# Optimization experiments

Hardware: AMD Instinct MI355X
Metric: run time of the kernel (lower is better)

Reference implementation:

```python
import jax, jax.numpy as jnp
import numpy as np

N = 50000    # nodes
E = 800000   # edges (avg degree 16)
B = 256      # graphs in the batch (static for segment ops)
H = 128      # feature / hidden width (channels[-2])
NL = 4       # LSTM layers in Set2Set
PS = 4       # Set2Set processing steps
OUT = 2      # channels[-1]


def _bn(h, g, b):
    # BatchNorm1d with batch statistics (training-mode math, biased variance)
    m = h.mean(0)
    v = jnp.mean((h - m) ** 2, 0)
    return (h - m) * jax.lax.rsqrt(v + 1e-5) * g + b


def _gin(x, src, dst, W1, b1, ga1, be1, W2, b2, ga2, be2):
    # GINConv, eps=0: out = MLP(x + sum_{j->i} x_j)
    agg = jax.ops.segment_sum(x[src], dst, num_segments=x.shape[0])
    h = x + agg
    h = jax.nn.relu(_bn(h @ W1.T + b1, ga1, be1))
    h = jax.nn.relu(_bn(h @ W2.T + b2, ga2, be2))
    return h


def _set2set(x, batch, Wih0, Whh0, b0, WihR, WhhR, bR):
    hs = [jnp.zeros((B, H), x.dtype)] * NL
    cs = [jnp.zeros((B, H), x.dtype)] * NL
    q_star = jnp.zeros((B, 2 * H), x.dtype)
    for _ in range(PS):
        inp = q_star
        nhs, ncs = [], []
        for l in range(NL):  # stacked LSTM cells, seq-len 1 per step
            Wih = Wih0 if l == 0 else WihR[l - 1]
            Whh = Whh0 if l == 0 else WhhR[l - 1]
            bb = b0 if l == 0 else bR[l - 1]
            gates = inp @ Wih.T + hs[l] @ Whh.T + bb
            i, f, g, o = jnp.split(gates, 4, axis=-1)  # torch gate order i,f,g,o
            c = jax.nn.sigmoid(f) * cs[l] + jax.nn.sigmoid(i) * jnp.tanh(g)
            h = jax.nn.sigmoid(o) * jnp.tanh(c)
            nhs.append(h); ncs.append(c)
            inp = h
        hs, cs = nhs, ncs
        q = inp  # (B, H) top-layer hidden
        # per-graph segment softmax attention
        e = jnp.sum(x * q[batch], -1)                        # (N,)
        m = jax.ops.segment_max(e, batch, num_segments=B)
        ee = jnp.exp(e - m[batch])
        s = jax.ops.segment_sum(ee, batch, num_segments=B)
        a = ee / s[batch]
        r = jax.ops.segment_sum(a[:, None] * x, batch, num_segments=B)  # (B, H)
        q_star = jnp.concatenate([q, r], -1)
    return q_star


def setup_inputs() -> dict:
    key = jax.random.key(0)
    ks = jax.random.split(key, 16)

    def w(k, shape):
        return jax.random.normal(k, shape, jnp.float32) * 0.05

    d = {}
    d["x"] = jax.random.normal(ks[0], (N, H), jnp.float32)
    d["edge_index"] = jax.random.randint(ks[1], (2, E), 0, N, dtype=jnp.int32)
    d["batch"] = jnp.sort(jax.random.randint(ks[2], (N,), 0, B, dtype=jnp.int32))
    for i, g in enumerate(("g0", "g1")):
        kk = jax.random.split(ks[3 + i], 2)
        d[g + "_W1"] = w(kk[0], (H, H)); d[g + "_b1"] = jnp.zeros((H,), jnp.float32)
        d[g + "_gamma1"] = jnp.ones((H,), jnp.float32); d[g + "_beta1"] = jnp.zeros((H,), jnp.float32)
        d[g + "_W2"] = w(kk[1], (H, H)); d[g + "_b2"] = jnp.zeros((H,), jnp.float32)
        d[g + "_gamma2"] = jnp.ones((H,), jnp.float32); d[g + "_beta2"] = jnp.zeros((H,), jnp.float32)
    d["Wih0"] = w(ks[6], (4 * H, 2 * H))
    d["Whh0"] = w(ks[7], (4 * H, H))
    d["b0"] = jnp.zeros((4 * H,), jnp.float32)
    d["WihR"] = w(ks[8], (NL - 1, 4 * H, H))
    d["WhhR"] = w(ks[9], (NL - 1, 4 * H, H))
    d["bR"] = jnp.zeros((NL - 1, 4 * H), jnp.float32)
    d["lin_W"] = w(ks[10], (OUT, 2 * H))
    d["lin_b"] = jnp.zeros((OUT,), jnp.float32)
    return d


def reference(x, edge_index, batch,
              g0_W1, g0_b1, g0_gamma1, g0_beta1, g0_W2, g0_b2, g0_gamma2, g0_beta2,
              g1_W1, g1_b1, g1_gamma1, g1_beta1, g1_W2, g1_b2, g1_gamma2, g1_beta2,
              Wih0, Whh0, b0, WihR, WhhR, bR, lin_W, lin_b):
    src, dst = edge_index[0], edge_index[1]
    x = _gin(x, src, dst, g0_W1, g0_b1, g0_gamma1, g0_beta1, g0_W2, g0_b2, g0_gamma2, g0_beta2)
    x = _gin(x, src, dst, g1_W1, g1_b1, g1_gamma1, g1_beta1, g1_W2, g1_b2, g1_gamma2, g1_beta2)
    q = _set2set(x, batch, Wih0, Whh0, b0, WihR, WhhR, bR)
    # F.dropout(p=0.1) is identity in eval mode
    return q @ lin_W.T + lin_b
```

## Files before the change

### kernel.cpp

```cpp
#include <hip/hip_runtime.h>
#include <math.h>

#define NN 50000
#define EE 800000
#define BBG 256
#define HHC 128
#define SEG_CAP 448
#define ESC 512
#define NBIN 196
#define NBLK 196

typedef _Float16 half8 __attribute__((ext_vector_type(8)));
typedef _Float16 half4 __attribute__((ext_vector_type(4)));
typedef _Float16 half2v __attribute__((ext_vector_type(2)));
typedef float f32x4 __attribute__((ext_vector_type(4)));

#if defined(__has_builtin)
#if __has_builtin(__builtin_amdgcn_fdot2)
#define USE_FDOT2 1
#endif
#endif

__device__ __forceinline__ float fdot2f(half2v a, half2v b, float c) {
#ifdef USE_FDOT2
  return __builtin_amdgcn_fdot2(a, b, c, false);
#else
  return fmaf((float)a[0], (float)b[0], fmaf((float)a[1], (float)b[1], c));
#endif
}

__device__ __forceinline__ float fsigm(float x) {
  return __builtin_amdgcn_rcpf(1.f + __expf(-x));
}
__device__ __forceinline__ float ftanh(float x) {
  return 1.f - 2.f * __builtin_amdgcn_rcpf(1.f + __expf(2.f * x));
}

__device__ __forceinline__ float4 aff4(float4 v, float4 sc, float4 sh) {
  v.x = fmaxf(fmaf(v.x, sc.x, sh.x), 0.f);
  v.y = fmaxf(fmaf(v.y, sc.y, sh.y), 0.f);
  v.z = fmaxf(fmaf(v.z, sc.z, sh.z), 0.f);
  v.w = fmaxf(fmaf(v.w, sc.w, sh.w), 0.f);
  return v;
}

__global__ __launch_bounds__(256) void prep_all_kernel(
    const int* __restrict__ batch,
    const int* __restrict__ ei,
    const float* __restrict__ W0, const float* __restrict__ W1,
    const float* __restrict__ W2, const float* __restrict__ W3,
    const float* __restrict__ Wih0, const float* __restrict__ Whh0,
    const float* __restrict__ WihR, const float* __restrict__ WhhR,
    const float* __restrict__ b0, const float* __restrict__ bR,
    const float* __restrict__ xsrc,
    float* __restrict__ stats, int* __restrict__ gptr, int* __restrict__ partial,
    _Float16* __restrict__ ginWh, _Float16* __restrict__ WT0h,
    _Float16* __restrict__ WTRh, float* __restrict__ bc0, float* __restrict__ bcR,
    _Float16* __restrict__ x16a) {
  __shared__ int hist[NBIN];
  int blk = blockIdx.x, tid = threadIdx.x;
  if (blk == 0) {
    ((float4*)stats)[tid] = make_float4(0.f, 0.f, 0.f, 0.f);
    return;
  }
  if (blk <= 196) {
    int i = (blk - 1) * 256 + tid;
    if (i >= NN) return;
    int b = batch[i];
    int prev = (i == 0) ? -1 : batch[i - 1];
    for (int g = prev + 1; g <= b; ++g) gptr[g] = i;
    if (i == NN - 1) {
      for (int g = b + 1; g <= BBG; ++g) gptr[g] = NN;
    }
    return;
  }
  if (blk <= 392) {
    int b = blk - 197;
    if (tid < NBIN) hist[tid] = 0;
    __syncthreads();
    const int4* dst4 = (const int4*)(ei + EE);
#pragma unroll
    for (int c = 0; c < 4; ++c) {
      int idx = b * 1024 + c * 256 + tid;
      if (idx < EE / 4) {
        int4 d = dst4[idx];
        atomicAdd(&hist[d.x >> 8], 1);
        atomicAdd(&hist[d.y >> 8], 1);
        atomicAdd(&hist[d.z >> 8], 1);
        atomicAdd(&hist[d.w >> 8], 1);
      }
    }
    __syncthreads();
    if (tid < NBIN) partial[tid * NBLK + b] = hist[tid];
    return;
  }
  if (blk >= 2961) {
    int i = (blk - 2961) * 256 + tid;
    float4 v = ((const float4*)xsrc)[i];
    half4 h;
    h[0] = (_Float16)v.x; h[1] = (_Float16)v.y;
    h[2] = (_Float16)v.z; h[3] = (_Float16)v.w;
    ((half4*)x16a)[i] = h;
    return;
  }
  int idx = (blk - 393) * 256 + tid;
  if (idx < 65536) {
    int m = idx >> 14;
    int r = idx & 16383;
    const float* W = (m == 0) ? W0 : (m == 1) ? W1 : (m == 2) ? W2 : W3;
    ginWh[idx] = (_Float16)W[r];
  } else if (idx < 262144) {
    int t = idx - 65536;
    int k = t >> 9, op = t & 511;
    int j = op >> 2, g = op & 3;
    int row = g * 128 + j;
    float v = (k < 256) ? Wih0[row * 256 + k] : Whh0[row * 128 + (k - 256)];
    WT0h[((k >> 1) << 10) | (op << 1) | (k & 1)] = (_Float16)v;
  } else if (idx < 655360) {
    int t = idx - 262144;
    int l = t >> 17;
    int rem = t & 131071;
    int k = rem >> 9, op = rem & 511;
    int j = op >> 2, g = op & 3;
    int row = g * 128 + j;
    float v = (k < 128) ? WihR[((size_t)l * 512 + row) * 128 + k]
                        : WhhR[((size_t)l * 512 + row) * 128 + (k - 128)];
    WTRh[((size_t)l << 17) | ((k >> 1) << 10) | (op << 1) | (k & 1)] = (_Float16)v;
  } else {
    int t = idx - 655360;
    if (t < 512) {
      bc0[t] = b0[(t & 3) * 128 + (t >> 2)];
    } else {
      int u = t - 512;
      int l = u >> 9, op = u & 511;
      bcR[u] = bR[l * 512 + (op & 3) * 128 + (op >> 2)];
    }
  }
}


__global__ void scan_partials_kernel(const int* __restrict__ partial,
                                     int* __restrict__ block_base, int* __restrict__ total) {
  __shared__ int buf[256];
  int bin = blockIdx.x, tid = threadIdx.x;
  int v = (tid < NBLK) ? partial[bin * NBLK + tid] : 0;
  buf[tid] = v;
  __syncthreads();
  for (int off = 1; off < 256; off <<= 1) {
    int t = (tid >= off) ? buf[tid - off] : 0;
    __syncthreads();
    buf[tid] += t;
    __syncthreads();
  }
  if (tid < NBLK) block_base[bin * NBLK + tid] = buf[tid] - v;
  if (tid == 255) total[bin] = buf[255];
}

__global__ void scan_totals_kernel(const int* __restrict__ total, int* __restrict__ coarse_base) {
  __shared__ int buf[256];
  int tid = threadIdx.x;
  int v = (tid < NBIN) ? total[tid] : 0;
  buf[tid] = v;
  __syncthreads();
  for (int off = 1; off < 256; off <<= 1) {
    int t = (tid >= off) ? buf[tid - off] : 0;
    __syncthreads();
    buf[tid] += t;
    __syncthreads();
  }
  if (tid < NBIN) coarse_base[tid] = buf[tid] - v;
  if (tid == 255) coarse_base[NBIN] = buf[255];
}

__global__ __launch_bounds__(256) void bucket_scatter_kernel(const int* __restrict__ ei,
                                                             const int* __restrict__ coarse_base,
                                                             const int* __restrict__ block_base,
                                                             int* __restrict__ packed) {
  __shared__ int cursor[NBIN];
  int tid = threadIdx.x, b = blockIdx.x;
  if (tid < NBIN) cursor[tid] = coarse_base[tid] + block_base[tid * NBLK + b];
  __syncthreads();
  const int4* src4 = (const int4*)ei;
  const int4* dst4 = (const int4*)(ei + EE);
#pragma unroll
  for (int c = 0; c < 4; ++c) {
    int idx = b * 1024 + c * 256 + tid;
    if (idx < EE / 4) {
      int4 s = src4[idx];
      int4 d = dst4[idx];
      int p;
      p = atomicAdd(&cursor[d.x >> 8], 1); packed[p] = (s.x << 8) | (d.x & 255);
      p = atomicAdd(&cursor[d.y >> 8], 1); packed[p] = (s.y << 8) | (d.y & 255);
      p = atomicAdd(&cursor[d.z >> 8], 1); packed[p] = (s.z << 8) | (d.z & 255);
      p = atomicAdd(&cursor[d.w >> 8], 1); packed[p] = (s.w << 8) | (d.w & 255);
    }
  }
}

__global__ __launch_bounds__(256) void csr_finalize_kernel(const int* __restrict__ packed,
                                                           const int* __restrict__ coarse_base,
                                                           int* __restrict__ row_start,
                                                           int* __restrict__ csr) {
  __shared__ int fh[256];
  __shared__ int fb[256];
  int bin = blockIdx.x, tid = threadIdx.x;
  int e0 = coarse_base[bin], e1 = coarse_base[bin + 1];
  fh[tid] = 0;
  __syncthreads();
  for (int e = e0 + tid; e < e1; e += 256) atomicAdd(&fh[packed[e] & 255], 1);
  __syncthreads();
  int v = fh[tid];
  fb[tid] = v;
  __syncthreads();
  for (int off = 1; off < 256; off <<= 1) {
    int t = (tid >= off) ? fb[tid - off] : 0;
    __syncthreads();
    fb[tid] += t;
    __syncthreads();
  }
  int excl = fb[tid] - v;
  int node = bin * 256 + tid;
  if (node < NN) row_start[node] = e0 + excl;
  if (bin == NBIN - 1 && tid == 0) row_start[NN] = EE;
  __syncthreads();
  fb[tid] = excl;
  __syncthreads();
  for (int e = e0 + tid; e < e1; e += 256) {
    int p = packed[e];
    int pos = atomicAdd(&fb[p & 255], 1);
    csr[e0 + pos] = p >> 8;
  }
}

template <bool AFF>
__device__ __forceinline__ void acc8(float* acc, half8 h, const float* scv,
                                     const float* shv) {
#pragma unroll
  for (int f = 0; f < 8; ++f) {
    float v = (float)h[f];
    if (AFF) v = fmaxf(fmaf(v, scv[f], shv[f]), 0.f);
    acc[f] += v;
  }
}

template <bool AFF>
__global__ __launch_bounds__(256) void gin_agg_kernel(
    const _Float16* __restrict__ x16, const int* __restrict__ row_start,
    const int* __restrict__ csr,
    const float* __restrict__ stats, const float* __restrict__ gamma,
    const float* __restrict__ beta, _Float16* __restrict__ outp) {
  __shared__ float sc_s[128], sh_s[128];
  if (AFF) {
    int tt = threadIdx.x;
    if (tt < 128) {
      const float invN = 1.0f / (float)NN;
      float mm = stats[tt] * invN;
      float vv = stats[128 + tt] * invN - mm * mm;
      float rs = rsqrtf(vv + 1e-5f);
      float sc = gamma[tt] * rs;
      sc_s[tt] = sc;
      sh_s[tt] = beta[tt] - mm * sc;
    }
    __syncthreads();
  }
  int node = blockIdx.x * 16 + (threadIdx.x >> 4);
  int t = threadIdx.x & 15;
  const half8* xh8 = (const half8*)x16;
  float scv[8], shv[8];
  if (AFF) {
#pragma unroll
    for (int f = 0; f < 8; ++f) { scv[f] = sc_s[t * 8 + f]; shv[f] = sh_s[t * 8 + f]; }
  }
  int s0 = row_start[node], s1 = row_start[node + 1];
  float acc[8] = {0.f, 0.f, 0.f, 0.f, 0.f, 0.f, 0.f, 0.f};
  int j = s0;
  for (; j + 8 <= s1; j += 8) {
    int i0 = csr[j + 0];
    int i1 = csr[j + 1];
    int i2 = csr[j + 2];
    int i3 = csr[j + 3];
    int i4 = csr[j + 4];
    int i5 = csr[j + 5];
    int i6 = csr[j + 6];
    int i7 = csr[j + 7];
    half8 h0 = xh8[(size_t)i0 * 16 + t];
    half8 h1 = xh8[(size_t)i1 * 16 + t];
    half8 h2 = xh8[(size_t)i2 * 16 + t];
    half8 h3 = xh8[(size_t)i3 * 16 + t];
    half8 h4 = xh8[(size_t)i4 * 16 + t];
    half8 h5 = xh8[(size_t)i5 * 16 + t];
    half8 h6 = xh8[(size_t)i6 * 16 + t];
    half8 h7 = xh8[(size_t)i7 * 16 + t];
    acc8<AFF>(acc, h0, scv, shv);
    acc8<AFF>(acc, h1, scv, shv);
    acc8<AFF>(acc, h2, scv, shv);
    acc8<AFF>(acc, h3, scv, shv);
    acc8<AFF>(acc, h4, scv, shv);
    acc8<AFF>(acc, h5, scv, shv);
    acc8<AFF>(acc, h6, scv, shv);
    acc8<AFF>(acc, h7, scv, shv);
  }
  if (j + 4 <= s1) {
    int i0 = csr[j + 0];
    int i1 = csr[j + 1];
    int i2 = csr[j + 2];
    int i3 = csr[j + 3];
    half8 h0 = xh8[(size_t)i0 * 16 + t];
    half8 h1 = xh8[(size_t)i1 * 16 + t];
    half8 h2 = xh8[(size_t)i2 * 16 + t];
    half8 h3 = xh8[(size_t)i3 * 16 + t];
    acc8<AFF>(acc, h0, scv, shv);
    acc8<AFF>(acc, h1, scv, shv);
    acc8<AFF>(acc, h2, scv, shv);
    acc8<AFF>(acc, h3, scv, shv);
    j += 4;
  }
  for (; j < s1; ++j) {
    int i = csr[j];
    half8 h = xh8[(size_t)i * 16 + t];
    acc8<AFF>(acc, h, scv, shv);
  }
  half8 selfh = xh8[(size_t)node * 16 + t];
  half8 hv;
#pragma unroll
  for (int f = 0; f < 8; ++f) {
    float sv = (float)selfh[f];
    if (AFF) sv = fmaxf(fmaf(sv, scv[f], shv[f]), 0.f);
    hv[f] = (_Float16)(acc[f] + sv);
  }
  ((half8*)outp)[(size_t)node * 16 + t] = hv;
}

template <bool BN, bool AH>
__global__ __launch_bounds__(256) void gemm_gin_mfma_kernel(
    const float* __restrict__ A, const _Float16* __restrict__ A16,
    const _Float16* __restrict__ Wh,
    const float* __restrict__ bias,
    const float* __restrict__ stats, const float* __restrict__ gamma,
    const float* __restrict__ beta,
    float* __restrict__ C, _Float16* __restrict__ h16out,
    float* __restrict__ ssum, float* __restrict__ ssq) {
  __shared__ float bsc_s[128], bsh_s[128];
  int tid = threadIdx.x;
  if (BN) {
    if (tid < 128) {
      const float invN = 1.0f / (float)NN;
      float mm = stats[tid] * invN;
      float vv = stats[128 + tid] * invN - mm * mm;
      float rs = rsqrtf(vv + 1e-5f);
      float sc = gamma[tid] * rs;
      bsc_s[tid] = sc;
      bsh_s[tid] = beta[tid] - mm * sc;
    }
    __syncthreads();
  }
  int w = tid >> 6, l = tid & 63;
  int lr = l & 15, lg = l >> 4;
  int cb = w * 32;
  half8 bf0[4], bf1[4];
#pragma unroll
  for (int ks = 0; ks < 4; ++ks) {
    int k = ks * 32 + lg * 8;
    bf0[ks] = *(const half8*)(Wh + (size_t)(cb + lr) * 128 + k);
    bf1[ks] = *(const half8*)(Wh + (size_t)(cb + 16 + lr) * 128 + k);
  }
  float bv0 = bias[cb + lr], bv1 = bias[cb + 16 + lr];
  float ps0 = 0.f, pq0 = 0.f, ps1 = 0.f, pq1 = 0.f;
  int t0 = blockIdx.x * 4;
  for (int t = 0; t < 4; ++t) {
    int tile = t0 + t;
    if (tile >= 3125) break;
    int r = tile * 16 + lr;
    half8 af[4];
#pragma unroll
    for (int ks = 0; ks < 4; ++ks) {
      int k0 = ks * 32 + lg * 8;
      if constexpr (AH) {
        half8 ah = *(const half8*)(A16 + (size_t)r * 128 + k0);
        if constexpr (BN) {
          float4 s0 = *(const float4*)&bsc_s[k0];
          float4 s1 = *(const float4*)&bsc_s[k0 + 4];
          float4 h0 = *(const float4*)&bsh_s[k0];
          float4 h1 = *(const float4*)&bsh_s[k0 + 4];
          half8 o;
          o[0] = (_Float16)fmaxf(fmaf((float)ah[0], s0.x, h0.x), 0.f);
          o[1] = (_Float16)fmaxf(fmaf((float)ah[1], s0.y, h0.y), 0.f);
          o[2] = (_Float16)fmaxf(fmaf((float)ah[2], s0.z, h0.z), 0.f);
          o[3] = (_Float16)fmaxf(fmaf((float)ah[3], s0.w, h0.w), 0.f);
          o[4] = (_Float16)fmaxf(fmaf((float)ah[4], s1.x, h1.x), 0.f);
          o[5] = (_Float16)fmaxf(fmaf((float)ah[5], s1.y, h1.y), 0.f);
          o[6] = (_Float16)fmaxf(fmaf((float)ah[6], s1.z, h1.z), 0.f);
          o[7] = (_Float16)fmaxf(fmaf((float)ah[7], s1.w, h1.w), 0.f);
          af[ks] = o;
        } else {
          af[ks] = ah;
        }
      } else {
        float4 a0 = *(const float4*)(A + (size_t)r * 128 + k0);
        float4 a1 = *(const float4*)(A + (size_t)r * 128 + k0 + 4);
        if constexpr (BN) {
          float4 s0 = *(const float4*)&bsc_s[k0];
          float4 s1 = *(const float4*)&bsc_s[k0 + 4];
          float4 h0 = *(const float4*)&bsh_s[k0];
          float4 h1 = *(const float4*)&bsh_s[k0 + 4];
          a0 = aff4(a0, s0, h0);
          a1 = aff4(a1, s1, h1);
        }
        half8 o;
        o[0] = (_Float16)a0.x; o[1] = (_Float16)a0.y;
        o[2] = (_Float16)a0.z; o[3] = (_Float16)a0.w;
        o[4] = (_Float16)a1.x; o[5] = (_Float16)a1.y;
        o[6] = (_Float16)a1.z; o[7] = (_Float16)a1.w;
        af[ks] = o;
      }
    }
    f32x4 acc0 = {0.f, 0.f, 0.f, 0.f};
    f32x4 acc1 = {0.f, 0.f, 0.f, 0.f};
#pragma unroll
    for (int ks = 0; ks < 4; ++ks) {
      acc0 = __builtin_amdgcn_mfma_f32_16x16x32_f16(af[ks], bf0[ks], acc0, 0, 0, 0);
      acc1 = __builtin_amdgcn_mfma_f32_16x16x32_f16(af[ks], bf1[ks], acc1, 0, 0, 0);
    }
#pragma unroll
    for (int i = 0; i < 4; ++i) {
      int rr = tile * 16 + lg * 4 + i;
      float v0 = acc0[i] + bv0;
      float v1 = acc1[i] + bv1;
      if (C) {
        C[(size_t)rr * 128 + cb + lr] = v0;
        C[(size_t)rr * 128 + cb + 16 + lr] = v1;
      }
      if (h16out) {
        h16out[(size_t)rr * 128 + cb + lr] = (_Float16)v0;
        h16out[(size_t)rr * 128 + cb + 16 + lr] = (_Float16)v1;
      }
      ps0 += v0; pq0 += v0 * v0;
      ps1 += v1; pq1 += v1 * v1;
    }
  }
  ps0 += __shfl_xor(ps0, 16); ps0 += __shfl_xor(ps0, 32);
  pq0 += __shfl_xor(pq0, 16); pq0 += __shfl_xor(pq0, 32);
  ps1 += __shfl_xor(ps1, 16); ps1 += __shfl_xor(ps1, 32);
  pq1 += __shfl_xor(pq1, 16); pq1 += __shfl_xor(pq1, 32);
  if (lg == 0) {
    atomicAdd(&ssum[cb + lr], ps0);
    atomicAdd(&ssq[cb + lr], pq0);
    atomicAdd(&ssum[cb + 16 + lr], ps1);
    atomicAdd(&ssq[cb + 16 + lr], pq1);
  }
}

__global__ void __launch_bounds__(1024) set2set_kernel(
    const _Float16* __restrict__ x, const int* __restrict__ gptr,
    const float* __restrict__ stats, const float* __restrict__ gamma,
    const float* __restrict__ beta,
    const _Float16* __restrict__ WT0h, const _Float16* __restrict__ WTRh,
    const float* __restrict__ bc0, const float* __restrict__ bcR,
    float* __restrict__ ebuf,
    const float* __restrict__ linW, const float* __restrict__ linb,
    float* __restrict__ out) {
  __shared__ half2v xs[SEG_CAP * 64];
  __shared__ float wpart[16][512];
  __shared__ half2v inp2[192];
  __shared__ float hcs[4][128];
  __shared__ float ccs[4][128];
  __shared__ float qst[256];
  __shared__ float es[ESC];
  __shared__ float bsc[128], bsh[128];
  __shared__ float wred[16];
  __shared__ float smax_s, ssum_s;
  __shared__ float fred[2][4];

  int g = blockIdx.x, tid = threadIdx.x;
  int w16 = tid >> 6, lane = tid & 63;

  if (tid < 128) {
    const float invN = 1.0f / (float)NN;
    float mm = stats[tid] * invN;
    float vv = stats[128 + tid] * invN - mm * mm;
    float rs = rsqrtf(vv + 1e-5f);
    float sc = gamma[tid] * rs;
    bsc[tid] = sc;
    bsh[tid] = beta[tid] - mm * sc;
#pragma unroll
    for (int l = 0; l < 4; ++l) { hcs[l][tid] = 0.f; ccs[l][tid] = 0.f; }
  }
  if (tid < 256) qst[tid] = 0.f;
  __syncthreads();

  int s0 = gptr[g], s1 = gptr[g + 1];
  int seg = s1 - s0;
  int ncache = seg < SEG_CAP ? seg : SEG_CAP;
  const half2v* xh = (const half2v*)x;
  float sc0 = bsc[2 * lane], sc1 = bsc[2 * lane + 1];
  float sh0 = bsh[2 * lane], sh1 = bsh[2 * lane + 1];
  for (int n = w16; n < ncache; n += 16) {
    half2v v = xh[(size_t)(s0 + n) * 64 + lane];
    half2v h;
    h[0] = (_Float16)fmaxf(fmaf((float)v[0], sc0, sh0), 0.f);
    h[1] = (_Float16)fmaxf(fmaf((float)v[1], sc1, sh1), 0.f);
    xs[n * 64 + lane] = h;
  }
  __syncthreads();

  int s_ = tid >> 6, cg = tid & 63;

  for (int step = 0; step < 4; ++step) {
    for (int cell = 0; cell < 4; ++cell) {
      const _Float16* WTh; const float* bias; int KP2;
      if (cell == 0) {
        WTh = WT0h; bias = bc0; KP2 = 12;
        if (tid < 192) {
          int k = tid << 1;
          float va, vb;
          if (k < 256) { va = qst[k]; vb = qst[k + 1]; }
          else { va = hcs[0][k - 256]; vb = hcs[0][k - 255]; }
          half2v h; h[0] = (_Float16)va; h[1] = (_Float16)vb;
          inp2[tid] = h;
        }
      } else {
        WTh = WTRh + (size_t)(cell - 1) * 131072;
        bias = bcR + (cell - 1) * 512; KP2 = 8;
        if (tid < 128) {
          int k = tid << 1;
          float va, vb;
          if (k < 128) { va = hcs[cell - 1][k]; vb = hcs[cell - 1][k + 1]; }
          else { va = hcs[cell][k - 128]; vb = hcs[cell][k - 127]; }
          half2v h; h[0] = (_Float16)va; h[1] = (_Float16)vb;
          inp2[tid] = h;
        }
      }
      __syncthreads();
      bool skipmv = (step == 0 && cell == 0);
      if (!skipmv) {
        int se = (s_ + g) & 15;
        int k20 = se * KP2;
        float a0 = 0.f, a1 = 0.f, a2 = 0.f, a3 = 0.f;
        float a4 = 0.f, a5 = 0.f, a6 = 0.f, a7 = 0.f;
        if (step != 0 || se < 8) {
          const char* wb = (const char*)WTh + (size_t)k20 * 2048 + (cg << 5);
#pragma unroll 4
          for (int k2 = 0; k2 < KP2; ++k2) {
            uint4 wa = *(const uint4*)(wb + (size_t)k2 * 2048);
            uint4 wc = *(const uint4*)(wb + (size_t)k2 * 2048 + 16);
            half2v i2 = inp2[k20 + k2];
            a0 = fdot2f(i2, __builtin_bit_cast(half2v, wa.x), a0);
            a1 = fdot2f(i2, __builtin_bit_cast(half2v, wa.y), a1);
            a2 = fdot2f(i2, __builtin_bit_cast(half2v, wa.z), a2);
            a3 = fdot2f(i2, __builtin_bit_cast(half2v, wa.w), a3);
            a4 = fdot2f(i2, __builtin_bit_cast(half2v, wc.x), a4);
            a5 = fdot2f(i2, __builtin_bit_cast(half2v, wc.y), a5);
            a6 = fdot2f(i2, __builtin_bit_cast(half2v, wc.z), a6);
            a7 = fdot2f(i2, __builtin_bit_cast(half2v, wc.w), a7);
          }
        }
        *(float4*)&wpart[s_][cg << 3] = make_float4(a0, a1, a2, a3);
        *(float4*)(&wpart[s_][cg << 3] + 4) = make_float4(a4, a5, a6, a7);
        __syncthreads();
      }
      if (tid < 128) {
        int j = tid;
        float4 ga = *(const float4*)&bias[4 * j];
        if (!skipmv) {
#pragma unroll
          for (int s = 0; s < 16; ++s) {
            float4 wv = *(const float4*)&wpart[s][4 * j];
            ga.x += wv.x; ga.y += wv.y; ga.z += wv.z; ga.w += wv.w;
          }
        }
        float cp = ccs[cell][j];
        float si = fsigm(ga.x);
        float sf = fsigm(ga.y);
        float so = fsigm(ga.w);
        float cn = sf * cp + si * ftanh(ga.z);
        ccs[cell][j] = cn;
        hcs[cell][j] = so * ftanh(cn);
      }
      __syncthreads();
    }
    float* rpart = &wpart[0][0];
    float qx = hcs[3][2 * lane], qy = hcs[3][2 * lane + 1];
    half2v q2; q2[0] = (_Float16)qx; q2[1] = (_Float16)qy;
    float wmax = -3.0e38f;
    for (int n = w16; n < seg; n += 16) {
      float e;
      if (n < ncache) {
        e = fdot2f(xs[n * 64 + lane], q2, 0.f);
      } else {
        half2v v = xh[(size_t)(s0 + n) * 64 + lane];
        float vx = fmaxf(fmaf((float)v[0], sc0, sh0), 0.f);
        float vy = fmaxf(fmaf((float)v[1], sc1, sh1), 0.f);
        e = vx * qx + vy * qy;
      }
#pragma unroll
      for (int sh = 32; sh; sh >>= 1) e += __shfl_xor(e, sh);
      if (lane == 0) { if (n < ESC) es[n] = e; else ebuf[s0 + n] = e; }
      wmax = fmaxf(wmax, e);
    }
    if (lane == 0) wred[w16] = wmax;
    __syncthreads();
    if (tid == 0) {
      float m = wred[0];
#pragma unroll
      for (int t = 1; t < 16; ++t) m = fmaxf(m, wred[t]);
      smax_s = m;
    }
    __syncthreads();
    float m = smax_s;
    float loc = 0.f;
    for (int n = tid; n < seg; n += 1024) {
      float e = (n < ESC) ? es[n] : ebuf[s0 + n];
      float ex = __expf(e - m);
      if (n < ESC) es[n] = ex; else ebuf[s0 + n] = ex;
      loc += ex;
    }
#pragma unroll
    for (int sh = 32; sh; sh >>= 1) loc += __shfl_xor(loc, sh);
    __syncthreads();
    if (lane == 0) wred[w16] = loc;
    __syncthreads();
    if (tid == 0) {
      float s = 0.f;
#pragma unroll
      for (int t = 0; t < 16; ++t) s += wred[t];
      ssum_s = s;
    }
    __syncthreads();
    float inv = 1.0f / ssum_s;
    float rx = 0.f, ry = 0.f;
    for (int n = w16; n < seg; n += 16) {
      float ex = (n < ESC) ? es[n] : ebuf[s0 + n];
      float coef = ex * inv;
      float vx, vy;
      if (n < ncache) {
        half2v v2 = xs[n * 64 + lane];
        vx = (float)v2[0]; vy = (float)v2[1];
      } else {
        half2v v = xh[(size_t)(s0 + n) * 64 + lane];
        vx = fmaxf(fmaf((float)v[0], sc0, sh0), 0.f);
        vy = fmaxf(fmaf((float)v[1], sc1, sh1), 0.f);
      }
      rx += coef * vx; ry += coef * vy;
    }
    rpart[w16 * 128 + 2 * lane] = rx;
    rpart[w16 * 128 + 2 * lane + 1] = ry;
    __syncthreads();
    if (tid < 128) {
      float r = 0.f;
#pragma unroll
      for (int t = 0; t < 16; ++t) r += rpart[t * 128 + tid];
      qst[tid] = hcs[3][tid];
      qst[128 + tid] = r;
    }
    __syncthreads();
  }
  if (tid < 256) {
    float val = qst[tid];
    float p0 = val * linW[tid];
    float p1 = val * linW[256 + tid];
#pragma unroll
    for (int sh = 32; sh; sh >>= 1) { p0 += __shfl_xor(p0, sh); p1 += __shfl_xor(p1, sh); }
    if (lane == 0) { fred[0][w16] = p0; fred[1][w16] = p1; }
  }
  __syncthreads();
  if (tid == 0) {
    out[2 * g + 0] = fred[0][0] + fred[0][1] + fred[0][2] + fred[0][3] + linb[0];
    out[2 * g + 1] = fred[1][0] + fred[1][1] + fred[1][2] + fred[1][3] + linb[1];
  }
}


extern "C" void kernel_launch(void* const* d_in, const int* in_sizes, int n_in,
                              void* d_out, int out_size, void* d_ws, size_t ws_size,
                              hipStream_t stream) {
  const float* x = (const float*)d_in[0];
  const int* ei = (const int*)d_in[1];
  const int* batch = (const int*)d_in[2];
  const float* gW[4]  = {(const float*)d_in[3],  (const float*)d_in[7],
                         (const float*)d_in[11], (const float*)d_in[15]};
  const float* gb[4]  = {(const float*)d_in[4],  (const float*)d_in[8],
                         (const float*)d_in[12], (const float*)d_in[16]};
  const float* gga[4] = {(const float*)d_in[5],  (const float*)d_in[9],
                         (const float*)d_in[13], (const float*)d_in[17]};
  const float* gbe[4] = {(const float*)d_in[6],  (const float*)d_in[10],
                         (const float*)d_in[14], (const float*)d_in[18]};
  const float* Wih0 = (const float*)d_in[19];
  const float* Whh0 = (const float*)d_in[20];
  const float* b0   = (const float*)d_in[21];
  const float* WihR = (const float*)d_in[22];
  const float* WhhR = (const float*)d_in[23];
  const float* bR   = (const float*)d_in[24];
  const float* linW = (const float*)d_in[25];
  const float* linb = (const float*)d_in[26];
  float* out = (float*)d_out;

  char* base = (char*)d_ws;
  size_t off = 0;
  auto allocf = [&](size_t n) { float* p = (float*)(base + off); off += n * sizeof(float); return p; };
  _Float16* agg16 = (_Float16*)(base + off); off += 6400000 * 2;
  _Float16* ginWh = (_Float16*)(base + off); off += 65536 * 2;
  _Float16* WT0h = (_Float16*)(base + off); off += 196608 * 2;
  _Float16* WTRh = (_Float16*)(base + off); off += 393216 * 2;
  _Float16* x16a = (_Float16*)(base + off); off += 6400000 * 2;
  _Float16* x16b = (_Float16*)(base + off); off += 6400000 * 2;
  float* bc0   = allocf(512);
  float* bcR   = allocf(1536);
  float* ebuf  = allocf(50000);
  float* stats = allocf(1024);
  int* row_start = (int*)(base + off); off += 50004 * 4;
  int* gptr = (int*)(base + off); off += 260 * 4;
  int* csr = (int*)(base + off); off += 800000 * 4;
  int* packed = (int*)(base + off); off += 800000 * 4;
  int* partial = (int*)(base + off); off += NBIN * NBLK * 4;
  int* block_base = (int*)(base + off); off += NBIN * NBLK * 4;
  int* total = (int*)(base + off); off += 256 * 4;
  int* coarse_base = (int*)(base + off); off += 260 * 4;
  (void)ws_size; (void)in_sizes; (void)n_in; (void)out_size;

  prep_all_kernel<<<9211, 256, 0, stream>>>(batch, ei, gW[0], gW[1], gW[2], gW[3],
                                            Wih0, Whh0, WihR, WhhR, b0, bR, x,
                                            stats, gptr, partial, ginWh, WT0h, WTRh,
                                            bc0, bcR, x16a);
  scan_partials_kernel<<<NBIN, 256, 0, stream>>>(partial, block_base, total);
  scan_totals_kernel<<<1, 256, 0, stream>>>(total, coarse_base);
  bucket_scatter_kernel<<<NBLK, 256, 0, stream>>>(ei, coarse_base, block_base, packed);
  csr_finalize_kernel<<<NBIN, 256, 0, stream>>>(packed, coarse_base, row_start, csr);

  gin_agg_kernel<false><<<3125, 256, 0, stream>>>(x16a, row_start, csr,
                                                  nullptr, nullptr, nullptr, agg16);
  gemm_gin_mfma_kernel<false, true><<<782, 256, 0, stream>>>(
      nullptr, agg16, ginWh + 0 * 16384, gb[0],
      nullptr, nullptr, nullptr,
      nullptr, x16a, stats + 0, stats + 128);
  gemm_gin_mfma_kernel<true, true><<<782, 256, 0, stream>>>(
      nullptr, x16a, ginWh + 1 * 16384, gb[1],
      stats + 0, gga[0], gbe[0],
      nullptr, x16b, stats + 256, stats + 384);
  gin_agg_kernel<true><<<3125, 256, 0, stream>>>(x16b, row_start, csr,
                                                 stats + 256, gga[1], gbe[1], agg16);
  gemm_gin_mfma_kernel<false, true><<<782, 256, 0, stream>>>(
      nullptr, agg16, ginWh + 2 * 16384, gb[2],
      nullptr, nullptr, nullptr,
      nullptr, x16a, stats + 512, stats + 640);
  gemm_gin_mfma_kernel<true, true><<<782, 256, 0, stream>>>(
      nullptr, x16a, ginWh + 3 * 16384, gb[3],
      stats + 512, gga[2], gbe[2],
      nullptr, x16b, stats + 768, stats + 896);

  set2set_kernel<<<256, 1024, 0, stream>>>(x16b, gptr, stats + 768, gga[3], gbe[3],
                                           WT0h, WTRh, bc0, bcR, ebuf, linW, linb, out);
}
```

Before: 424.2 us.

## Fuse GIN neighbor aggregation with first MLP GEMM and fold totals scan into consumers

Each GIN layer's sparse aggregation now writes its 16-node tiles into shared memory and runs the first MFMA GEMM in the same kernel, so the aggregated fp16 intermediate no longer round-trips through global memory. The single-block scan of bin totals is removed and recomputed redundantly inside the scatter and finalize kernels, saving one launch. The unaffine aggregation sums are regrouped as pairwise trees, and the unused fp32 GEMM path is dropped. In exchange, the fused kernel launches 4x fewer blocks, each doing more serial gather work, which may lower the latency hiding for irregular gathers.

Result: faster. 409.2 us (-3.5%).

```diff
diff --git a/kernel.cpp b/kernel.cpp
--- a/kernel.cpp
+++ b/kernel.cpp
@@ -156,29 +156,23 @@
   if (tid == 255) total[bin] = buf[255];
 }
 
-__global__ void scan_totals_kernel(const int* __restrict__ total, int* __restrict__ coarse_base) {
-  __shared__ int buf[256];
-  int tid = threadIdx.x;
-  int v = (tid < NBIN) ? total[tid] : 0;
-  buf[tid] = v;
-  __syncthreads();
-  for (int off = 1; off < 256; off <<= 1) {
-    int t = (tid >= off) ? buf[tid - off] : 0;
-    __syncthreads();
-    buf[tid] += t;
-    __syncthreads();
-  }
-  if (tid < NBIN) coarse_base[tid] = buf[tid] - v;
-  if (tid == 255) coarse_base[NBIN] = buf[255];
-}
-
 __global__ __launch_bounds__(256) void bucket_scatter_kernel(const int* __restrict__ ei,
-                                                             const int* __restrict__ coarse_base,
+                                                             const int* __restrict__ total,
                                                              const int* __restrict__ block_base,
                                                              int* __restrict__ packed) {
+  __shared__ int sbuf[256];
   __shared__ int cursor[NBIN];
   int tid = threadIdx.x, b = blockIdx.x;
-  if (tid < NBIN) cursor[tid] = coarse_base[tid] + block_base[tid * NBLK + b];
+  int v = (tid < NBIN) ? total[tid] : 0;
+  sbuf[tid] = v;
+  __syncthreads();
+  for (int off = 1; off < 256; off <<= 1) {
+    int t = (tid >= off) ? sbuf[tid - off] : 0;
+    __syncthreads();
+    sbuf[tid] += t;
+    __syncthreads();
+  }
+  if (tid < NBIN) cursor[tid] = (sbuf[tid] - v) + block_base[tid * NBLK + b];
   __syncthreads();
   const int4* src4 = (const int4*)ei;
   const int4* dst4 = (const int4*)(ei + EE);
@@ -198,13 +192,24 @@
 }
 
 __global__ __launch_bounds__(256) void csr_finalize_kernel(const int* __restrict__ packed,
-                                                           const int* __restrict__ coarse_base,
+                                                           const int* __restrict__ total,
                                                            int* __restrict__ row_start,
                                                            int* __restrict__ csr) {
   __shared__ int fh[256];
   __shared__ int fb[256];
   int bin = blockIdx.x, tid = threadIdx.x;
-  int e0 = coarse_base[bin], e1 = coarse_base[bin + 1];
+  int tv = (tid < NBIN) ? total[tid] : 0;
+  fb[tid] = tv;
+  __syncthreads();
+  for (int off = 1; off < 256; off <<= 1) {
+    int t = (tid >= off) ? fb[tid - off] : 0;
+    __syncthreads();
+    fb[tid] += t;
+    __syncthreads();
+  }
+  int e0 = (bin == 0) ? 0 : fb[bin - 1];
+  int e1 = fb[bin];
+  __syncthreads();
   fh[tid] = 0;
   __syncthreads();
   for (int e = e0 + tid; e < e1; e += 256) atomicAdd(&fh[packed[e] & 255], 1);
@@ -233,112 +238,182 @@
 }
 
 template <bool AFF>
-__device__ __forceinline__ void acc8(float* acc, half8 h, const float* scv,
-                                     const float* shv) {
-#pragma unroll
-  for (int f = 0; f < 8; ++f) {
-    float v = (float)h[f];
-    if (AFF) v = fmaxf(fmaf(v, scv[f], shv[f]), 0.f);
-    acc[f] += v;
-  }
-}
-
-template <bool AFF>
-__global__ __launch_bounds__(256) void gin_agg_kernel(
+__global__ __launch_bounds__(256) void agg_gemm_kernel(
     const _Float16* __restrict__ x16, const int* __restrict__ row_start,
     const int* __restrict__ csr,
     const float* __restrict__ stats, const float* __restrict__ gamma,
-    const float* __restrict__ beta, _Float16* __restrict__ outp) {
+    const float* __restrict__ beta,
+    const _Float16* __restrict__ Wh, const float* __restrict__ bias,
+    _Float16* __restrict__ h16out,
+    float* __restrict__ ssum, float* __restrict__ ssq) {
+  __shared__ _Float16 As[4][16][136];
   __shared__ float sc_s[128], sh_s[128];
+  int tid = threadIdx.x;
   if (AFF) {
-    int tt = threadIdx.x;
-    if (tt < 128) {
+    if (tid < 128) {
       const float invN = 1.0f / (float)NN;
-      float mm = stats[tt] * invN;
-      float vv = stats[128 + tt] * invN - mm * mm;
+      float mm = stats[tid] * invN;
+      float vv = stats[128 + tid] * invN - mm * mm;
       float rs = rsqrtf(vv + 1e-5f);
-      float sc = gamma[tt] * rs;
-      sc_s[tt] = sc;
-      sh_s[tt] = beta[tt] - mm * sc;
-    }
-    __syncthreads();
-  }
-  int node = blockIdx.x * 16 + (threadIdx.x >> 4);
-  int t = threadIdx.x & 15;
-  const half8* xh8 = (const half8*)x16;
-  float scv[8], shv[8];
-  if (AFF) {
-#pragma unroll
-    for (int f = 0; f < 8; ++f) { scv[f] = sc_s[t * 8 + f]; shv[f] = sh_s[t * 8 + f]; }
-  }
-  int s0 = row_start[node], s1 = row_start[node + 1];
-  float acc[8] = {0.f, 0.f, 0.f, 0.f, 0.f, 0.f, 0.f, 0.f};
-  int j = s0;
-  for (; j + 8 <= s1; j += 8) {
-    int i0 = csr[j + 0];
-    int i1 = csr[j + 1];
-    int i2 = csr[j + 2];
-    int i3 = csr[j + 3];
-    int i4 = csr[j + 4];
-    int i5 = csr[j + 5];
-    int i6 = csr[j + 6];
-    int i7 = csr[j + 7];
-    half8 h0 = xh8[(size_t)i0 * 16 + t];
-    half8 h1 = xh8[(size_t)i1 * 16 + t];
-    half8 h2 = xh8[(size_t)i2 * 16 + t];
-    half8 h3 = xh8[(size_t)i3 * 16 + t];
-    half8 h4 = xh8[(size_t)i4 * 16 + t];
-    half8 h5 = xh8[(size_t)i5 * 16 + t];
-    half8 h6 = xh8[(size_t)i6 * 16 + t];
-    half8 h7 = xh8[(size_t)i7 * 16 + t];
-    acc8<AFF>(acc, h0, scv, shv);
-    acc8<AFF>(acc, h1, scv, shv);
-    acc8<AFF>(acc, h2, scv, shv);
-    acc8<AFF>(acc, h3, scv, shv);
-    acc8<AFF>(acc, h4, scv, shv);
-    acc8<AFF>(acc, h5, scv, shv);
-    acc8<AFF>(acc, h6, scv, shv);
-    acc8<AFF>(acc, h7, scv, shv);
-  }
-  if (j + 4 <= s1) {
-    int i0 = csr[j + 0];
-    int i1 = csr[j + 1];
-    int i2 = csr[j + 2];
-    int i3 = csr[j + 3];
-    half8 h0 = xh8[(size_t)i0 * 16 + t];
-    half8 h1 = xh8[(size_t)i1 * 16 + t];
-    half8 h2 = xh8[(size_t)i2 * 16 + t];
-    half8 h3 = xh8[(size_t)i3 * 16 + t];
-    acc8<AFF>(acc, h0, scv, shv);
-    acc8<AFF>(acc, h1, scv, shv);
-    acc8<AFF>(acc, h2, scv, shv);
-    acc8<AFF>(acc, h3, scv, shv);
-    j += 4;
-  }
-  for (; j < s1; ++j) {
-    int i = csr[j];
-    half8 h = xh8[(size_t)i * 16 + t];
-    acc8<AFF>(acc, h, scv, shv);
-  }
-  half8 selfh = xh8[(size_t)node * 16 + t];
-  half8 hv;
-#pragma unroll
-  for (int f = 0; f < 8; ++f) {
-    float sv = (float)selfh[f];
-    if (AFF) sv = fmaxf(fmaf(sv, scv[f], shv[f]), 0.f);
-    hv[f] = (_Float16)(acc[f] + sv);
-  }
-  ((half8*)outp)[(size_t)node * 16 + t] = hv;
-}
-
-template <bool BN, bool AH>
+      float sc = gamma[tid] * rs;
+      sc_s[tid] = sc;
+      sh_s[tid] = beta[tid] - mm * sc;
+    }
+    __syncthreads();
+  }
+  int tile0 = blockIdx.x * 4;
+  {
+    int nloc = tid >> 4;
+    int t = tid & 15;
+    const half8* xh8 = (const half8*)x16;
+    float scv[8], shv[8];
+    if (AFF) {
+#pragma unroll
+      for (int f = 0; f < 8; ++f) { scv[f] = sc_s[t * 8 + f]; shv[f] = sh_s[t * 8 + f]; }
+    }
+    for (int tt = 0; tt < 4; ++tt) {
+      int tile = tile0 + tt;
+      if (tile >= 3125) break;
+      int node = tile * 16 + nloc;
+      int s0 = row_start[node], s1 = row_start[node + 1];
+      float acc[8] = {0.f, 0.f, 0.f, 0.f, 0.f, 0.f, 0.f, 0.f};
+      int j = s0;
+      for (; j + 8 <= s1; j += 8) {
+        int i0 = csr[j + 0];
+        int i1 = csr[j + 1];
+        int i2 = csr[j + 2];
+        int i3 = csr[j + 3];
+        int i4 = csr[j + 4];
+        int i5 = csr[j + 5];
+        int i6 = csr[j + 6];
+        int i7 = csr[j + 7];
+        half8 h0 = xh8[(size_t)i0 * 16 + t];
+        half8 h1 = xh8[(size_t)i1 * 16 + t];
+        half8 h2 = xh8[(size_t)i2 * 16 + t];
+        half8 h3 = xh8[(size_t)i3 * 16 + t];
+        half8 h4 = xh8[(size_t)i4 * 16 + t];
+        half8 h5 = xh8[(size_t)i5 * 16 + t];
+        half8 h6 = xh8[(size_t)i6 * 16 + t];
+        half8 h7 = xh8[(size_t)i7 * 16 + t];
+#pragma unroll
+        for (int f = 0; f < 8; ++f) {
+          if (AFF) {
+            acc[f] += fmaxf(fmaf((float)h0[f], scv[f], shv[f]), 0.f);
+            acc[f] += fmaxf(fmaf((float)h1[f], scv[f], shv[f]), 0.f);
+            acc[f] += fmaxf(fmaf((float)h2[f], scv[f], shv[f]), 0.f);
+            acc[f] += fmaxf(fmaf((float)h3[f], scv[f], shv[f]), 0.f);
+            acc[f] += fmaxf(fmaf((float)h4[f], scv[f], shv[f]), 0.f);
+            acc[f] += fmaxf(fmaf((float)h5[f], scv[f], shv[f]), 0.f);
+            acc[f] += fmaxf(fmaf((float)h6[f], scv[f], shv[f]), 0.f);
+            acc[f] += fmaxf(fmaf((float)h7[f], scv[f], shv[f]), 0.f);
+          } else {
+            acc[f] += (((float)h0[f] + (float)h1[f]) + ((float)h2[f] + (float)h3[f])) +
+                      (((float)h4[f] + (float)h5[f]) + ((float)h6[f] + (float)h7[f]));
+          }
+        }
+      }
+      if (j + 4 <= s1) {
+        int i0 = csr[j + 0];
+        int i1 = csr[j + 1];
+        int i2 = csr[j + 2];
+        int i3 = csr[j + 3];
+        half8 h0 = xh8[(size_t)i0 * 16 + t];
+        half8 h1 = xh8[(size_t)i1 * 16 + t];
+        half8 h2 = xh8[(size_t)i2 * 16 + t];
+        half8 h3 = xh8[(size_t)i3 * 16 + t];
+#pragma unroll
+        for (int f = 0; f < 8; ++f) {
+          if (AFF) {
+            acc[f] += fmaxf(fmaf((float)h0[f], scv[f], shv[f]), 0.f);
+            acc[f] += fmaxf(fmaf((float)h1[f], scv[f], shv[f]), 0.f);
+            acc[f] += fmaxf(fmaf((float)h2[f], scv[f], shv[f]), 0.f);
+            acc[f] += fmaxf(fmaf((float)h3[f], scv[f], shv[f]), 0.f);
+          } else {
+            acc[f] += ((float)h0[f] + (float)h1[f]) + ((float)h2[f] + (float)h3[f]);
+          }
+        }
+        j += 4;
+      }
+      for (; j < s1; ++j) {
+        int i = csr[j];
+        half8 h = xh8[(size_t)i * 16 + t];
+#pragma unroll
+        for (int f = 0; f < 8; ++f) {
+          float v = (float)h[f];
+          if (AFF) v = fmaxf(fmaf(v, scv[f], shv[f]), 0.f);
+          acc[f] += v;
+        }
+      }
+      half8 selfh = xh8[(size_t)node * 16 + t];
+      half8 hv;
+#pragma unroll
+      for (int f = 0; f < 8; ++f) {
+        float sv = (float)selfh[f];
+        if (AFF) sv = fmaxf(fmaf(sv, scv[f], shv[f]), 0.f);
+        hv[f] = (_Float16)(acc[f] + sv);
+      }
+      *(half8*)&As[tt][nloc][t * 8] = hv;
+    }
+  }
+  __syncthreads();
+  int w = tid >> 6, l = tid & 63;
+  int lr = l & 15, lg = l >> 4;
+  int cb = w * 32;
+  half8 bf0[4], bf1[4];
+#pragma unroll
+  for (int ks = 0; ks < 4; ++ks) {
+    int k = ks * 32 + lg * 8;
+    bf0[ks] = *(const half8*)(Wh + (size_t)(cb + lr) * 128 + k);
+    bf1[ks] = *(const half8*)(Wh + (size_t)(cb + 16 + lr) * 128 + k);
+  }
+  float bv0 = bias[cb + lr], bv1 = bias[cb + 16 + lr];
+  float ps0 = 0.f, pq0 = 0.f, ps1 = 0.f, pq1 = 0.f;
+  for (int tt = 0; tt < 4; ++tt) {
+    int tile = tile0 + tt;
+    if (tile >= 3125) break;
+    half8 af[4];
+#pragma unroll
+    for (int ks = 0; ks < 4; ++ks) {
+      af[ks] = *(const half8*)&As[tt][lr][ks * 32 + lg * 8];
+    }
+    f32x4 acc0 = {0.f, 0.f, 0.f, 0.f};
+    f32x4 acc1 = {0.f, 0.f, 0.f, 0.f};
+#pragma unroll
+    for (int ks = 0; ks < 4; ++ks) {
+      acc0 = __builtin_amdgcn_mfma_f32_16x16x32_f16(af[ks], bf0[ks], acc0, 0, 0, 0);
+      acc1 = __builtin_amdgcn_mfma_f32_16x16x32_f16(af[ks], bf1[ks], acc1, 0, 0, 0);
+    }
+#pragma unroll
+    for (int i = 0; i < 4; ++i) {
+      int rr = tile * 16 + lg * 4 + i;
+      float v0 = acc0[i] + bv0;
+      float v1 = acc1[i] + bv1;
+      h16out[(size_t)rr * 128 + cb + lr] = (_Float16)v0;
+      h16out[(size_t)rr * 128 + cb + 16 + lr] = (_Float16)v1;
+      ps0 += v0; pq0 += v0 * v0;
+      ps1 += v1; pq1 += v1 * v1;
+    }
+  }
+  ps0 += __shfl_xor(ps0, 16); ps0 += __shfl_xor(ps0, 32);
+  pq0 += __shfl_xor(pq0, 16); pq0 += __shfl_xor(pq0, 32);
+  ps1 += __shfl_xor(ps1, 16); ps1 += __shfl_xor(ps1, 32);
+  pq1 += __shfl_xor(pq1, 16); pq1 += __shfl_xor(pq1, 32);
+  if (lg == 0) {
+    atomicAdd(&ssum[cb + lr], ps0);
+    atomicAdd(&ssq[cb + lr], pq0);
+    atomicAdd(&ssum[cb + 16 + lr], ps1);
+    atomicAdd(&ssq[cb + 16 + lr], pq1);
+  }
+}
+
+template <bool BN>
 __global__ __launch_bounds__(256) void gemm_gin_mfma_kernel(
-    const float* __restrict__ A, const _Float16* __restrict__ A16,
+    const _Float16* __restrict__ A16,
     const _Float16* __restrict__ Wh,
     const float* __restrict__ bias,
     const float* __restrict__ stats, const float* __restrict__ gamma,
     const float* __restrict__ beta,
-    float* __restrict__ C, _Float16* __restrict__ h16out,
+    _Float16* __restrict__ h16out,
     float* __restrict__ ssum, float* __restrict__ ssq) {
   __shared__ float bsc_s[128], bsh_s[128];
   int tid = threadIdx.x;
@@ -375,43 +450,24 @@
 #pragma unroll
     for (int ks = 0; ks < 4; ++ks) {
       int k0 = ks * 32 + lg * 8;
-      if constexpr (AH) {
-        half8 ah = *(const half8*)(A16 + (size_t)r * 128 + k0);
-        if constexpr (BN) {
-          float4 s0 = *(const float4*)&bsc_s[k0];
-          float4 s1 = *(const float4*)&bsc_s[k0 + 4];
-          float4 h0 = *(const float4*)&bsh_s[k0];
-          float4 h1 = *(const float4*)&bsh_s[k0 + 4];
-          half8 o;
-          o[0] = (_Float16)fmaxf(fmaf((float)ah[0], s0.x, h0.x), 0.f);
-          o[1] = (_Float16)fmaxf(fmaf((float)ah[1], s0.y, h0.y), 0.f);
-          o[2] = (_Float16)fmaxf(fmaf((float)ah[2], s0.z, h0.z), 0.f);
-          o[3] = (_Float16)fmaxf(fmaf((float)ah[3], s0.w, h0.w), 0.f);
-          o[4] = (_Float16)fmaxf(fmaf((float)ah[4], s1.x, h1.x), 0.f);
-          o[5] = (_Float16)fmaxf(fmaf((float)ah[5], s1.y, h1.y), 0.f);
-          o[6] = (_Float16)fmaxf(fmaf((float)ah[6], s1.z, h1.z), 0.f);
-          o[7] = (_Float16)fmaxf(fmaf((float)ah[7], s1.w, h1.w), 0.f);
-          af[ks] = o;
-        } else {
-          af[ks] = ah;
-        }
+      half8 ah = *(const half8*)(A16 + (size_t)r * 128 + k0);
+      if constexpr (BN) {
+        float4 s0 = *(const float4*)&bsc_s[k0];
+        float4 s1 = *(const float4*)&bsc_s[k0 + 4];
+        float4 h0 = *(const float4*)&bsh_s[k0];
+        float4 h1 = *(const float4*)&bsh_s[k0 + 4];
+        half8 o;
+        o[0] = (_Float16)fmaxf(fmaf((float)ah[0], s0.x, h0.x), 0.f);
+        o[1] = (_Float16)fmaxf(fmaf((float)ah[1], s0.y, h0.y), 0.f);
+        o[2] = (_Float16)fmaxf(fmaf((float)ah[2], s0.z, h0.z), 0.f);
+        o[3] = (_Float16)fmaxf(fmaf((float)ah[3], s0.w, h0.w), 0.f);
+        o[4] = (_Float16)fmaxf(fmaf((float)ah[4], s1.x, h1.x), 0.f);
+        o[5] = (_Float16)fmaxf(fmaf((float)ah[5], s1.y, h1.y), 0.f);
+        o[6] = (_Float16)fmaxf(fmaf((float)ah[6], s1.z, h1.z), 0.f);
+        o[7] = (_Float16)fmaxf(fmaf((float)ah[7], s1.w, h1.w), 0.f);
+        af[ks] = o;
       } else {
-        float4 a0 = *(const float4*)(A + (size_t)r * 128 + k0);
-        float4 a1 = *(const float4*)(A + (size_t)r * 128 + k0 + 4);
-        if constexpr (BN) {
-          float4 s0 = *(const float4*)&bsc_s[k0];
-          float4 s1 = *(const float4*)&bsc_s[k0 + 4];
-          float4 h0 = *(const float4*)&bsh_s[k0];
-          float4 h1 = *(const float4*)&bsh_s[k0 + 4];
-          a0 = aff4(a0, s0, h0);
-          a1 = aff4(a1, s1, h1);
-        }
-        half8 o;
-        o[0] = (_Float16)a0.x; o[1] = (_Float16)a0.y;
-        o[2] = (_Float16)a0.z; o[3] = (_Float16)a0.w;
-        o[4] = (_Float16)a1.x; o[5] = (_Float16)a1.y;
-        o[6] = (_Float16)a1.z; o[7] = (_Float16)a1.w;
-        af[ks] = o;
+        af[ks] = ah;
       }
     }
     f32x4 acc0 = {0.f, 0.f, 0.f, 0.f};
@@ -426,14 +482,8 @@
       int rr = tile * 16 + lg * 4 + i;
       float v0 = acc0[i] + bv0;
       float v1 = acc1[i] + bv1;
-      if (C) {
-        C[(size_t)rr * 128 + cb + lr] = v0;
-        C[(size_t)rr * 128 + cb + 16 + lr] = v1;
-      }
-      if (h16out) {
-        h16out[(size_t)rr * 128 + cb + lr] = (_Float16)v0;
-        h16out[(size_t)rr * 128 + cb + 16 + lr] = (_Float16)v1;
-      }
+      h16out[(size_t)rr * 128 + cb + lr] = (_Float16)v0;
+      h16out[(size_t)rr * 128 + cb + 16 + lr] = (_Float16)v1;
       ps0 += v0; pq0 += v0 * v0;
       ps1 += v1; pq1 += v1 * v1;
     }
@@ -697,12 +747,12 @@
   char* base = (char*)d_ws;
   size_t off = 0;
   auto allocf = [&](size_t n) { float* p = (float*)(base + off); off += n * sizeof(float); return p; };
-  _Float16* agg16 = (_Float16*)(base + off); off += 6400000 * 2;
+  _Float16* bufA = (_Float16*)(base + off); off += 6400000 * 2;
+  _Float16* bufB = (_Float16*)(base + off); off += 6400000 * 2;
+  _Float16* bufC = (_Float16*)(base + off); off += 6400000 * 2;
   _Float16* ginWh = (_Float16*)(base + off); off += 65536 * 2;
   _Float16* WT0h = (_Float16*)(base + off); off += 196608 * 2;
   _Float16* WTRh = (_Float16*)(base + off); off += 393216 * 2;
-  _Float16* x16a = (_Float16*)(base + off); off += 6400000 * 2;
-  _Float16* x16b = (_Float16*)(base + off); off += 6400000 * 2;
   float* bc0   = allocf(512);
   float* bcR   = allocf(1536);
   float* ebuf  = allocf(50000);
@@ -714,39 +764,35 @@
   int* partial = (int*)(base + off); off += NBIN * NBLK * 4;
   int* block_base = (int*)(base + off); off += NBIN * NBLK * 4;
   int* total = (int*)(base + off); off += 256 * 4;
-  int* coarse_base = (int*)(base + off); off += 260 * 4;
   (void)ws_size; (void)in_sizes; (void)n_in; (void)out_size;
 
   prep_all_kernel<<<9211, 256, 0, stream>>>(batch, ei, gW[0], gW[1], gW[2], gW[3],
                                             Wih0, Whh0, WihR, WhhR, b0, bR, x,
                                             stats, gptr, partial, ginWh, WT0h, WTRh,
-                                            bc0, bcR, x16a);
+                                            bc0, bcR, bufA);
   scan_partials_kernel<<<NBIN, 256, 0, stream>>>(partial, block_base, total);
-  scan_totals_kernel<<<1, 256, 0, stream>>>(total, coarse_base);
-  bucket_scatter_kernel<<<NBLK, 256, 0, stream>>>(ei, coarse_base, block_base, packed);
-  csr_finalize_kernel<<<NBIN, 256, 0, stream>>>(packed, coarse_base, row_start, csr);
-
-  gin_agg_kernel<false><<<3125, 256, 0, stream>>>(x16a, row_start, csr,
-                                                  nullptr, nullptr, nullptr, agg16);
-  gemm_gin_mfma_kernel<false, true><<<782, 256, 0, stream>>>(
-      nullptr, agg16, ginWh + 0 * 16384, gb[0],
+  bucket_scatter_kernel<<<NBLK, 256, 0, stream>>>(ei, total, block_base, packed);
+  csr_finalize_kernel<<<NBIN, 256, 0, stream>>>(packed, total, row_start, csr);
+
+  agg_gemm_kernel<false><<<782, 256, 0, stream>>>(
+      bufA, row_start, csr,
       nullptr, nullptr, nullptr,
-      nullptr, x16a, stats + 0, stats + 128);
-  gemm_gin_mfma_kernel<true, true><<<782, 256, 0, stream>>>(
-      nullptr, x16a, ginWh + 1 * 16384, gb[1],
+      ginWh + 0 * 16384, gb[0],
+      bufB, stats + 0, stats + 128);
+  gemm_gin_mfma_kernel<true><<<782, 256, 0, stream>>>(
+      bufB, ginWh + 1 * 16384, gb[1],
       stats + 0, gga[0], gbe[0],
-      nullptr, x16b, stats + 256, stats + 384);
-  gin_agg_kernel<true><<<3125, 256, 0, stream>>>(x16b, row_start, csr,
-                                                 stats + 256, gga[1], gbe[1], agg16);
-  gemm_gin_mfma_kernel<false, true><<<782, 256, 0, stream>>>(
-      nullptr, agg16, ginWh + 2 * 16384, gb[2],
-      nullptr, nullptr, nullptr,
-      nullptr, x16a, stats + 512, stats + 640);
-  gemm_gin_mfma_kernel<true, true><<<782, 256, 0, stream>>>(
-      nullptr, x16a, ginWh + 3 * 16384, gb[3],
+      bufC, stats + 256, stats + 384);
+  agg_gemm_kernel<true><<<782, 256, 0, stream>>>(
+      bufC, row_start, csr,
+      stats + 256, gga[1], gbe[1],
+      ginWh + 2 * 16384, gb[2],
+      bufB, stats + 512, stats + 640);
+  gemm_gin_mfma_kernel<true><<<782, 256, 0, stream>>>(
+      bufB, ginWh + 3 * 16384, gb[3],
       stats + 512, gga[2], gbe[2],
-      nullptr, x16b, stats + 768, stats + 896);
-
-  set2set_kernel<<<256, 1024, 0, stream>>>(x16b, gptr, stats + 768, gga[3], gbe[3],
+      bufA, stats + 768, stats + 896);
+
+  set2set_kernel<<<256, 1024, 0, stream>>>(bufA, gptr, stats + 768, gga[3], gbe[3],
                                            WT0h, WTRh, bc0, bcR, ebuf, linW, linb, out);
 }
```
